# Kernel tuning notes

Measured on AMD Instinct MI355X. Metric: run time of the kernel, lower is better.

The kernel has to match this reference:

```python
import jax, jax.numpy as jnp
import numpy as np

# R-FCN PSRoI pooling constants (match init_kwargs)
P = 7          # pooled_height == pooled_width
GS = 7         # group_size
D = 21         # output_dim
SCALE = 0.0625 # spatial_scale (1/16)


def setup_inputs() -> dict:
    key = jax.random.key(0)
    k1, k2, k3, k4 = jax.random.split(key, 4)
    N, C, H, W = 4, D * GS * GS, 80, 80   # C = output_dim * group_size^2
    R = 2048
    features = jax.random.normal(k1, (N, C, H, W), dtype=jnp.float32)
    img = H / SCALE  # 1280 px image
    bidx = jax.random.randint(k2, (R,), 0, N).astype(jnp.float32)
    xy1 = jax.random.uniform(k3, (R, 2), minval=0.0, maxval=img * 0.6)
    wh = jax.random.uniform(k4, (R, 2), minval=img * 0.05, maxval=img * 0.4)
    xy2 = jnp.clip(xy1 + wh, 0.0, img - 1.0)
    rois = jnp.concatenate([bidx[:, None], xy1, xy2], axis=1)  # [R,5]: (b,x1,y1,x2,y2)
    return {"features": features, "rois": rois}


def reference(features, rois):
    """Position-sensitive RoI pooling (R-FCN psroi_pooling_forward_cuda semantics).

    Each output bin (ctop, ph, pw) averages feature channel
    c = (ctop*GS + gh)*GS + gw over the bin's integer pixel region.
    Bin sums are computed exactly via a 2D integral image, turning the
    irregular per-bin reduction into 4 gathers per bin.
    """
    N, C, H, W = features.shape
    R = rois.shape[0]

    # Integral image: ii[n,c,i,j] = sum of features[n,c,:i,:j]; shape [N,C,H+1,W+1]
    ii = jnp.pad(
        jnp.cumsum(jnp.cumsum(features, axis=2), axis=3),
        ((0, 0), (0, 0), (1, 0), (1, 0)),
    )

    b = rois[:, 0].astype(jnp.int32)                       # [R]
    x1 = jnp.round(rois[:, 1]) * SCALE
    y1 = jnp.round(rois[:, 2]) * SCALE
    x2 = (jnp.round(rois[:, 3]) + 1.0) * SCALE
    y2 = (jnp.round(rois[:, 4]) + 1.0) * SCALE
    bin_w = jnp.maximum(x2 - x1, 0.1) / P                  # [R]
    bin_h = jnp.maximum(y2 - y1, 0.1) / P

    g = jnp.arange(P, dtype=jnp.float32)                   # bin index grid
    hs = jnp.clip(jnp.floor(g[None, :] * bin_h[:, None] + y1[:, None]), 0, H).astype(jnp.int32)        # [R,P]
    he = jnp.clip(jnp.ceil((g[None, :] + 1.0) * bin_h[:, None] + y1[:, None]), 0, H).astype(jnp.int32)
    ws = jnp.clip(jnp.floor(g[None, :] * bin_w[:, None] + x1[:, None]), 0, W).astype(jnp.int32)
    we = jnp.clip(jnp.ceil((g[None, :] + 1.0) * bin_w[:, None] + x1[:, None]), 0, W).astype(jnp.int32)

    # Position-sensitive channel map: c[ctop,ph,pw] = (ctop*GS+gh)*GS+gw
    ctop = jnp.arange(D)[:, None, None]
    gh = jnp.clip((jnp.arange(P) * GS) // P, 0, GS - 1)[None, :, None]
    gw = jnp.clip((jnp.arange(P) * GS) // P, 0, GS - 1)[None, None, :]
    cmap = (ctop * GS + gh) * GS + gw                      # [D,P,P]

    # Broadcast gather indices to [R,D,P,P]
    B = b[:, None, None, None]
    Cc = cmap[None]
    HS = hs[:, None, :, None]; HE = he[:, None, :, None]
    WS = ws[:, None, None, :]; WE = we[:, None, None, :]

    s = ii[B, Cc, HE, WE] - ii[B, Cc, HS, WE] - ii[B, Cc, HE, WS] + ii[B, Cc, HS, WS]
    area = ((HE - HS) * (WE - WS)).astype(features.dtype)
    out = jnp.where(area > 0, s / jnp.maximum(area, 1.0), jnp.zeros((), features.dtype))
    return out  # [R, D, P, P]
```

## Files before the change

kernel.cpp:

```cpp
#include <hip/hip_runtime.h>

#define P   7
#define GS  7
#define D   21
#define HH  80
#define WW  80
#define CC  (D * GS * GS)
#define PLANE (HH * WW)
#define IW  84
#define NSEG 5
#define SEGLEN 16
#define NBLK 512
#define BUFQ 2048
#define BUFF (BUFQ * 4)
#define REALQ 1680

__device__ __forceinline__ float recip7() {
    union { unsigned u; float f; } c; c.u = 0x3E124925u; return c.f;
}

__device__ __forceinline__ float mul_add_nofma(float a, float b, float c) {
    float t = a * b;
    asm volatile("" : "+v"(t));
    return t + c;
}

#define MEMFENCE() asm volatile("" ::: "memory")
#define LGKM_BAR() do { asm volatile("s_waitcnt lgkmcnt(0)" ::: "memory"); \
                        __builtin_amdgcn_s_barrier(); MEMFENCE(); } while (0)

__device__ __forceinline__ void gll16(const float* g, float* l) {
    __builtin_amdgcn_global_load_lds(
        (const __attribute__((address_space(1))) void*)g,
        (__attribute__((address_space(3))) void*)l, 16, 0, 0);
}

__device__ __forceinline__ void stage_issue(const float* plane, float* buf, int tid) {
    #pragma unroll
    for (int k = 0; k < 4; ++k) {
        int q0 = (tid & ~63) + k * 512;
        int q  = q0 + (tid & 63);
        int row = q / 21, w4 = q - row * 21;
        const float* src = (q < REALQ && w4 < 20) ? (plane + row * WW + w4 * 4)
                                                  : plane;
        gll16(src, buf + q0 * 4);
    }
}

__global__ __launch_bounds__(1024) void prep_kernel(
    const float* __restrict__ rois, int R, int N,
    unsigned short* __restrict__ hshe,
    unsigned short* __restrict__ wswe,
    int* __restrict__ jlist, int* __restrict__ base)
{
    __shared__ unsigned char bsh[2048];
    __shared__ int wcnt[16][8];
    __shared__ int wbase[16][8];
    __shared__ int baseS[9];
    int tid = threadIdx.x, wave = tid >> 6, lane = tid & 63;

    for (int r = tid; r < R; r += 1024) {
        const float* roi = rois + (size_t)r * 5;
        bsh[r] = (unsigned char)(int)roi[0];

        float x1 = rintf(roi[1]) * 0.0625f;
        float y1 = rintf(roi[2]) * 0.0625f;
        float x2 = (rintf(roi[3]) + 1.0f) * 0.0625f;
        float y2 = (rintf(roi[4]) + 1.0f) * 0.0625f;
        float bin_w = fmaxf(x2 - x1, 0.1f) * recip7();
        float bin_h = fmaxf(y2 - y1, 0.1f) * recip7();
        asm volatile("" : "+v"(bin_w), "+v"(bin_h));

        #pragma unroll
        for (int g = 0; g < 7; ++g) {
            float hs_f = floorf(mul_add_nofma((float)g,       bin_h, y1));
            float he_f = ceilf (mul_add_nofma((float)(g + 1), bin_h, y1));
            float ws_f = floorf(mul_add_nofma((float)g,       bin_w, x1));
            float we_f = ceilf (mul_add_nofma((float)(g + 1), bin_w, x1));
            int hs = (int)fminf(fmaxf(hs_f, 0.0f), 80.0f);
            int he = (int)fminf(fmaxf(he_f, 0.0f), 80.0f);
            int ws = (int)fminf(fmaxf(ws_f, 0.0f), 80.0f);
            int we = (int)fminf(fmaxf(we_f, 0.0f), 80.0f);
            hshe[r * 7 + g] = (unsigned short)(hs | (he << 8));
            wswe[r * 7 + g] = (unsigned short)(ws | (we << 8));
        }
    }
    __syncthreads();

    int chunk = (R + 15) / 16;
    int rbeg = wave * chunk;
    int rend = min(rbeg + chunk, R);
    int cnt[8];
    #pragma unroll
    for (int b = 0; b < 8; ++b) cnt[b] = 0;
    for (int rr = rbeg + lane; rr < rend; rr += 64) {
        int bv = bsh[rr];
        #pragma unroll
        for (int b = 0; b < 8; ++b) {
            if (b < N) cnt[b] += __popcll(__ballot(bv == b));
        }
    }
    if (lane == 0) {
        #pragma unroll
        for (int b = 0; b < 8; ++b) wcnt[wave][b] = cnt[b];
    }
    __syncthreads();

    if (tid < 8) {
        int b = tid, acc = 0;
        for (int w = 0; w < 16; ++w) { wbase[w][b] = acc; acc += wcnt[w][b]; }
        baseS[b] = acc;
    }
    __syncthreads();
    if (tid == 0) {
        int acc = 0;
        for (int b = 0; b < N; ++b) { int t = baseS[b]; baseS[b] = acc; acc += t; }
        baseS[N] = acc;
    }
    __syncthreads();

    {
        int off[8];
        #pragma unroll
        for (int b = 0; b < 8; ++b) off[b] = (b < N) ? (baseS[b] + wbase[wave][b]) : 0;
        for (int rr = rbeg + lane; rr < rend; rr += 64) {
            int bv = bsh[rr];
            #pragma unroll
            for (int b = 0; b < 8; ++b) {
                if (b < N) {
                    unsigned long long mask = __ballot(bv == b);
                    if (bv == b) {
                        int pos = off[b] + __popcll(mask & ((1ull << lane) - 1ull));
                        jlist[pos] = rr;
                    }
                    off[b] += __popcll(mask);
                }
            }
        }
    }
    if (tid <= N) base[tid] = baseS[tid];
}

__global__ __launch_bounds__(512) void psroi_plane_kernel(
    const float* __restrict__ feat, int R, int NPLANES,
    const unsigned short* __restrict__ hshe,
    const unsigned short* __restrict__ wswe,
    const int* __restrict__ jlist, const int* __restrict__ base,
    float* __restrict__ dst)
{
    __shared__ float bufA[BUFF];
    __shared__ float bufB[BUFF];
    __shared__ float tot[NSEG][HH];

    int tid = threadIdx.x;
    int bid = blockIdx.x;

    stage_issue(feat + (size_t)bid * PLANE, bufA, tid);

    bool act = tid < NSEG * WW;
    int seg = tid / WW;
    int lw  = tid % WW;

    int parity = 0;
    for (int p = bid; p < NPLANES; p += NBLK, parity ^= 1) {
        float* ii = parity ? bufB : bufA;
        float* nx = parity ? bufA : bufB;
        int pn = p + NBLK;
        if (pn < NPLANES) {
            stage_issue(feat + (size_t)pn * PLANE, nx, tid);
            asm volatile("s_waitcnt vmcnt(4)" ::: "memory");
        } else {
            asm volatile("s_waitcnt vmcnt(0)" ::: "memory");
        }
        __builtin_amdgcn_s_barrier();
        MEMFENCE();

        int b = p / CC, c = p % CC;
        int rem = c % (GS * GS);
        int gh  = rem / GS, gw = rem % GS;
        int j0 = base[b], j1 = base[b + 1];
        int jA = j0 + tid, jB = jA + 512, jC = jA + 1024, jD = jA + 1536;
        int rA = (jA < j1) ? jlist[jA] : 0;
        int rB = (jB < j1) ? jlist[jB] : 0;
        int rC = (jC < j1) ? jlist[jC] : 0;
        int rD = (jD < j1) ? jlist[jD] : 0;
        unsigned hA = (jA < j1) ? hshe[rA * 7 + gh] : 0;
        unsigned wA = (jA < j1) ? wswe[rA * 7 + gw] : 0;
        unsigned hB = (jB < j1) ? hshe[rB * 7 + gh] : 0;
        unsigned wB = (jB < j1) ? wswe[rB * 7 + gw] : 0;
        unsigned hC = (jC < j1) ? hshe[rC * 7 + gh] : 0;
        unsigned wC = (jC < j1) ? wswe[rC * 7 + gw] : 0;
        unsigned hD = (jD < j1) ? hshe[rD * 7 + gh] : 0;
        unsigned wD = (jD < j1) ? wswe[rD * 7 + gw] : 0;

        {
            float v[SEGLEN];
            int col = lw, h0 = seg * SEGLEN;
            if (act) {
                float s = 0.0f;
                #pragma unroll
                for (int k = 0; k < SEGLEN; ++k) { v[k] = ii[(h0 + k) * IW + col]; s += v[k]; }
                tot[seg][lw] = s;
            }
            LGKM_BAR();
            if (act) {
                float off = 0.0f;
                #pragma unroll
                for (int jj = 0; jj < NSEG - 1; ++jj) if (jj < seg) off += tot[jj][lw];
                float run = off;
                #pragma unroll
                for (int k = 0; k < SEGLEN; ++k) { run += v[k]; ii[(h0 + k) * IW + col] = run; }
            }
            LGKM_BAR();
        }
        {
            float4 q0, q1, q2, q3;
            int row = lw, w0 = seg * SEGLEN;
            float4* rp = (float4*)&ii[row * IW + w0];
            if (act) {
                q0 = rp[0]; q1 = rp[1]; q2 = rp[2]; q3 = rp[3];
                float s;
                s  = q0.x; s += q0.y; s += q0.z; s += q0.w;
                s += q1.x; s += q1.y; s += q1.z; s += q1.w;
                s += q2.x; s += q2.y; s += q2.z; s += q2.w;
                s += q3.x; s += q3.y; s += q3.z; s += q3.w;
                tot[seg][row] = s;
            }
            LGKM_BAR();
            if (act) {
                float off = 0.0f;
                #pragma unroll
                for (int jj = 0; jj < NSEG - 1; ++jj) if (jj < seg) off += tot[jj][row];
                float run = off;
                run += q0.x; q0.x = run; run += q0.y; q0.y = run;
                run += q0.z; q0.z = run; run += q0.w; q0.w = run;
                run += q1.x; q1.x = run; run += q1.y; q1.y = run;
                run += q1.z; q1.z = run; run += q1.w; q1.w = run;
                run += q2.x; q2.x = run; run += q2.y; q2.y = run;
                run += q2.z; q2.z = run; run += q2.w; q2.w = run;
                run += q3.x; q3.x = run; run += q3.y; q3.y = run;
                run += q3.z; q3.z = run; run += q3.w; q3.w = run;
                rp[0] = q0; rp[1] = q1; rp[2] = q2; rp[3] = q3;
            }
            LGKM_BAR();
        }

        #define IIV(hq, wq) ( ((hq) > 0 && (wq) > 0)                              \
            ? ii[((hq) - 1) * IW + ((wq) - 1)] : 0.0f )
        #define EMIT(jX, hX, wX)                                                  \
        if (jX < j1) {                                                            \
            int hs = hX & 255, he = (int)(hX >> 8);                               \
            int ws = wX & 255, we = (int)(wX >> 8);                               \
            float s = ((IIV(he, we) - IIV(hs, we))                                \
                     -  IIV(he, ws)) + IIV(hs, ws);                               \
            int area = (he - hs) * (we - ws);                                     \
            dst[(size_t)c * R + jX] = (area > 0) ? (s / (float)area) : 0.0f;      \
        }
        EMIT(jA, hA, wA)
        EMIT(jB, hB, wB)
        EMIT(jC, hC, wC)
        EMIT(jD, hD, wD)
        #undef EMIT
        #undef IIV

        LGKM_BAR();
    }
}

__global__ __launch_bounds__(256) void transpose_kernel(
    const float* __restrict__ in, const int* __restrict__ jlist,
    float* __restrict__ out, int R, int C)
{
    __shared__ float t[64][65];
    __shared__ int rows[64];
    int j0 = blockIdx.x * 64;
    int c0 = blockIdx.y * 64;
    int tx = threadIdx.x, ty = threadIdx.y;
    int tid = ty * 64 + tx;

    if (tid < 64 && j0 + tid < R) rows[tid] = jlist[j0 + tid];

    #pragma unroll
    for (int k0 = 0; k0 < 64; k0 += 4) {
        int k = k0 + ty;
        int cc = c0 + k, jj = j0 + tx;
        if (cc < C && jj < R) t[k][tx] = in[(size_t)cc * R + jj];
    }
    __syncthreads();
    #pragma unroll
    for (int k0 = 0; k0 < 64; k0 += 4) {
        int k = k0 + ty;
        int cc = c0 + tx;
        if (j0 + k < R && cc < C) out[(size_t)rows[k] * C + cc] = t[tx][k];
    }
}

__global__ __launch_bounds__(256) void psroi_fallback_kernel(
    const float* __restrict__ feat, const float* __restrict__ rois,
    int R, float* __restrict__ out)
{
    __shared__ float ii[81 * 81];
    int bid = blockIdx.x;
    int b = bid / CC, c = bid % CC;
    int rem = c % 49, gh = rem / 7, gw = rem % 7;

    const float* plane = feat + ((size_t)b * CC + c) * PLANE;
    for (int i = threadIdx.x; i < PLANE; i += 256) {
        int h = i / WW, w = i % WW;
        ii[(h + 1) * 81 + (w + 1)] = plane[i];
    }
    for (int i = threadIdx.x; i < 81; i += 256) { ii[i] = 0.0f; ii[i * 81] = 0.0f; }
    __syncthreads();
    if (threadIdx.x < WW) {
        int w = threadIdx.x + 1; float s = 0.0f;
        for (int h = 1; h <= HH; ++h) { s += ii[h * 81 + w]; ii[h * 81 + w] = s; }
    }
    __syncthreads();
    if (threadIdx.x < HH) {
        int h = threadIdx.x + 1; float* row = &ii[h * 81]; float s = 0.0f;
        for (int w = 1; w <= WW; ++w) { s += row[w]; row[w] = s; }
    }
    __syncthreads();
    for (int r = threadIdx.x; r < R; r += 256) {
        const float* roi = rois + (size_t)r * 5;
        if ((int)roi[0] != b) continue;
        float x1 = rintf(roi[1]) * 0.0625f;
        float y1 = rintf(roi[2]) * 0.0625f;
        float x2 = (rintf(roi[3]) + 1.0f) * 0.0625f;
        float y2 = (rintf(roi[4]) + 1.0f) * 0.0625f;
        float bw = fmaxf(x2 - x1, 0.1f) * recip7();
        float bh = fmaxf(y2 - y1, 0.1f) * recip7();
        asm volatile("" : "+v"(bw), "+v"(bh));
        int hs = (int)fminf(fmaxf(floorf(mul_add_nofma((float)gh,     bh, y1)), 0.0f), 80.0f);
        int he = (int)fminf(fmaxf(ceilf (mul_add_nofma((float)(gh+1), bh, y1)), 0.0f), 80.0f);
        int ws = (int)fminf(fmaxf(floorf(mul_add_nofma((float)gw,     bw, x1)), 0.0f), 80.0f);
        int we = (int)fminf(fmaxf(ceilf (mul_add_nofma((float)(gw+1), bw, x1)), 0.0f), 80.0f);
        float s = ii[he * 81 + we] - ii[hs * 81 + we] - ii[he * 81 + ws] + ii[hs * 81 + ws];
        int area = (he - hs) * (we - ws);
        out[(size_t)r * CC + c] = (area > 0) ? (s / (float)area) : 0.0f;
    }
}

extern "C" void kernel_launch(void* const* d_in, const int* in_sizes, int n_in,
                              void* d_out, int out_size, void* d_ws, size_t ws_size,
                              hipStream_t stream)
{
    const float* feat = (const float*)d_in[0];
    const float* rois = (const float*)d_in[1];
    float* out        = (float*)d_out;

    int R = in_sizes[1] / 5;
    int N = in_sizes[0] / (CC * PLANE);
    int NPLANES = N * CC;

    size_t off_wsT  = 0;
    size_t off_hshe = (off_wsT + (size_t)CC * R * sizeof(float) + 15) & ~(size_t)15;
    size_t off_wswe = off_hshe + (size_t)R * 7 * sizeof(unsigned short);
    size_t off_jl   = (off_wswe + (size_t)R * 7 * sizeof(unsigned short) + 15) & ~(size_t)15;
    size_t off_base = off_jl + (size_t)R * sizeof(int);
    size_t need     = off_base + (size_t)(N + 1) * sizeof(int);

    bool chunk_ok = (((R + 15) / 16) % 64) == 0;

    if (ws_size >= need && N <= 8 && R <= 2048 && chunk_ok && NPLANES > NBLK) {
        char* ws = (char*)d_ws;
        float*          ws_T = (float*)(ws + off_wsT);
        unsigned short* hshe = (unsigned short*)(ws + off_hshe);
        unsigned short* wswe = (unsigned short*)(ws + off_wswe);
        int*            jl   = (int*)(ws + off_jl);
        int*            base = (int*)(ws + off_base);

        prep_kernel<<<1, 1024, 0, stream>>>(rois, R, N, hshe, wswe, jl, base);
        psroi_plane_kernel<<<NBLK, 512, 0, stream>>>(
            feat, R, NPLANES, hshe, wswe, jl, base, ws_T);
        dim3 blk(64, 4), grd((R + 63) / 64, (CC + 63) / 64);
        transpose_kernel<<<grd, blk, 0, stream>>>(ws_T, jl, out, R, CC);
    } else {
        psroi_fallback_kernel<<<NPLANES, 256, 0, stream>>>(feat, rois, R, out);
    }
}
```

Before: 51.78 us.

## Replace LDS double-buffer async loads with register prefetch and single LDS plane

Drops the two LDS plane buffers filled by global_load_lds and instead prefetches the next plane into registers during compute, writing it to a single LDS buffer after the current plane's emit phase. Halving LDS use and adding launch_bounds(512,6) aims to raise occupancy, and the persistent grid grows from 512 to 768 blocks. The cost is higher register pressure and an extra barrier plus LDS write per plane, and the global loads now cannot land directly in LDS.

After: 54.10 us. 1.04x slower.

```diff
diff --git a/kernel.cpp b/kernel.cpp
--- a/kernel.cpp
+++ b/kernel.cpp
@@ -10,10 +10,8 @@
 #define IW  84
 #define NSEG 5
 #define SEGLEN 16
-#define NBLK 512
-#define BUFQ 2048
-#define BUFF (BUFQ * 4)
-#define REALQ 1680
+#define GRIDB 768
+#define Q4N 144
 
 __device__ __forceinline__ float recip7() {
     union { unsigned u; float f; } c; c.u = 0x3E124925u; return c.f;
@@ -28,24 +26,6 @@
 #define MEMFENCE() asm volatile("" ::: "memory")
 #define LGKM_BAR() do { asm volatile("s_waitcnt lgkmcnt(0)" ::: "memory"); \
                         __builtin_amdgcn_s_barrier(); MEMFENCE(); } while (0)
-
-__device__ __forceinline__ void gll16(const float* g, float* l) {
-    __builtin_amdgcn_global_load_lds(
-        (const __attribute__((address_space(1))) void*)g,
-        (__attribute__((address_space(3))) void*)l, 16, 0, 0);
-}
-
-__device__ __forceinline__ void stage_issue(const float* plane, float* buf, int tid) {
-    #pragma unroll
-    for (int k = 0; k < 4; ++k) {
-        int q0 = (tid & ~63) + k * 512;
-        int q  = q0 + (tid & 63);
-        int row = q / 21, w4 = q - row * 21;
-        const float* src = (q < REALQ && w4 < 20) ? (plane + row * WW + w4 * 4)
-                                                  : plane;
-        gll16(src, buf + q0 * 4);
-    }
-}
 
 __global__ __launch_bounds__(1024) void prep_kernel(
     const float* __restrict__ rois, int R, int N,
@@ -141,39 +121,59 @@
     if (tid <= N) base[tid] = baseS[tid];
 }
 
-__global__ __launch_bounds__(512) void psroi_plane_kernel(
+__global__ __launch_bounds__(512, 6) void psroi_plane_kernel(
     const float* __restrict__ feat, int R, int NPLANES,
     const unsigned short* __restrict__ hshe,
     const unsigned short* __restrict__ wswe,
     const int* __restrict__ jlist, const int* __restrict__ base,
     float* __restrict__ dst)
 {
-    __shared__ float bufA[BUFF];
-    __shared__ float bufB[BUFF];
+    __shared__ float ii[HH * IW];
     __shared__ float tot[NSEG][HH];
 
     int tid = threadIdx.x;
     int bid = blockIdx.x;
-
-    stage_issue(feat + (size_t)bid * PLANE, bufA, tid);
+    bool s4 = tid < Q4N;
+
+    int q0 = tid, q1 = tid + 512, q2 = tid + 1024, q3 = tid + 1536;
+    int r0_ = q0 / 21, c40 = q0 - r0_ * 21;
+    int r1_ = q1 / 21, c41 = q1 - r1_ * 21;
+    int r2_ = q2 / 21, c42 = q2 - r2_ * 21;
+    int r3_ = q3 / 21, c43 = q3 - r3_ * 21;
+    int g0 = (c40 < 20) ? (r0_ * WW + c40 * 4) : 0;
+    int g1 = (c41 < 20) ? (r1_ * WW + c41 * 4) : 0;
+    int g2 = (c42 < 20) ? (r2_ * WW + c42 * 4) : 0;
+    int g3 = (c43 < 20) ? (r3_ * WW + c43 * 4) : 0;
 
     bool act = tid < NSEG * WW;
     int seg = tid / WW;
     int lw  = tid % WW;
 
-    int parity = 0;
-    for (int p = bid; p < NPLANES; p += NBLK, parity ^= 1) {
-        float* ii = parity ? bufB : bufA;
-        float* nx = parity ? bufA : bufB;
-        int pn = p + NBLK;
-        if (pn < NPLANES) {
-            stage_issue(feat + (size_t)pn * PLANE, nx, tid);
-            asm volatile("s_waitcnt vmcnt(4)" ::: "memory");
-        } else {
-            asm volatile("s_waitcnt vmcnt(0)" ::: "memory");
-        }
-        __builtin_amdgcn_s_barrier();
-        MEMFENCE();
+    {
+        const float* pl = feat + (size_t)bid * PLANE;
+        float4 a0 = *(const float4*)(pl + g0);
+        float4 a1 = *(const float4*)(pl + g1);
+        float4 a2 = *(const float4*)(pl + g2);
+        float4 a3 = s4 ? *(const float4*)(pl + g3) : make_float4(0, 0, 0, 0);
+        *(float4*)(ii + q0 * 4) = a0;
+        *(float4*)(ii + q1 * 4) = a1;
+        *(float4*)(ii + q2 * 4) = a2;
+        if (s4) *(float4*)(ii + q3 * 4) = a3;
+    }
+    LGKM_BAR();
+
+    for (int p = bid; p < NPLANES; p += GRIDB) {
+        int pn = p + GRIDB;
+        bool has_next = pn < NPLANES;
+
+        float4 n0, n1, n2, n3;
+        {
+            const float* pl = feat + (size_t)(has_next ? pn : p) * PLANE;
+            n0 = *(const float4*)(pl + g0);
+            n1 = *(const float4*)(pl + g1);
+            n2 = *(const float4*)(pl + g2);
+            n3 = s4 ? *(const float4*)(pl + g3) : make_float4(0, 0, 0, 0);
+        }
 
         int b = p / CC, c = p % CC;
         int rem = c % (GS * GS);
@@ -214,16 +214,16 @@
             LGKM_BAR();
         }
         {
-            float4 q0, q1, q2, q3;
-            int row = lw, w0 = seg * SEGLEN;
-            float4* rp = (float4*)&ii[row * IW + w0];
+            float4 q4a, q4b, q4c, q4d;
+            int row = lw, w0s = seg * SEGLEN;
+            float4* rp = (float4*)&ii[row * IW + w0s];
             if (act) {
-                q0 = rp[0]; q1 = rp[1]; q2 = rp[2]; q3 = rp[3];
+                q4a = rp[0]; q4b = rp[1]; q4c = rp[2]; q4d = rp[3];
                 float s;
-                s  = q0.x; s += q0.y; s += q0.z; s += q0.w;
-                s += q1.x; s += q1.y; s += q1.z; s += q1.w;
-                s += q2.x; s += q2.y; s += q2.z; s += q2.w;
-                s += q3.x; s += q3.y; s += q3.z; s += q3.w;
+                s  = q4a.x; s += q4a.y; s += q4a.z; s += q4a.w;
+                s += q4b.x; s += q4b.y; s += q4b.z; s += q4b.w;
+                s += q4c.x; s += q4c.y; s += q4c.z; s += q4c.w;
+                s += q4d.x; s += q4d.y; s += q4d.z; s += q4d.w;
                 tot[seg][row] = s;
             }
             LGKM_BAR();
@@ -232,15 +232,15 @@
                 #pragma unroll
                 for (int jj = 0; jj < NSEG - 1; ++jj) if (jj < seg) off += tot[jj][row];
                 float run = off;
-                run += q0.x; q0.x = run; run += q0.y; q0.y = run;
-                run += q0.z; q0.z = run; run += q0.w; q0.w = run;
-                run += q1.x; q1.x = run; run += q1.y; q1.y = run;
-                run += q1.z; q1.z = run; run += q1.w; q1.w = run;
-                run += q2.x; q2.x = run; run += q2.y; q2.y = run;
-                run += q2.z; q2.z = run; run += q2.w; q2.w = run;
-                run += q3.x; q3.x = run; run += q3.y; q3.y = run;
-                run += q3.z; q3.z = run; run += q3.w; q3.w = run;
-                rp[0] = q0; rp[1] = q1; rp[2] = q2; rp[3] = q3;
+                run += q4a.x; q4a.x = run; run += q4a.y; q4a.y = run;
+                run += q4a.z; q4a.z = run; run += q4a.w; q4a.w = run;
+                run += q4b.x; q4b.x = run; run += q4b.y; q4b.y = run;
+                run += q4b.z; q4b.z = run; run += q4b.w; q4b.w = run;
+                run += q4c.x; q4c.x = run; run += q4c.y; q4c.y = run;
+                run += q4c.z; q4c.z = run; run += q4c.w; q4c.w = run;
+                run += q4d.x; q4d.x = run; run += q4d.y; q4d.y = run;
+                run += q4d.z; q4d.z = run; run += q4d.w; q4d.w = run;
+                rp[0] = q4a; rp[1] = q4b; rp[2] = q4c; rp[3] = q4d;
             }
             LGKM_BAR();
         }
@@ -263,6 +263,14 @@
         #undef EMIT
         #undef IIV
 
+        LGKM_BAR();
+
+        if (has_next) {
+            *(float4*)(ii + q0 * 4) = n0;
+            *(float4*)(ii + q1 * 4) = n1;
+            *(float4*)(ii + q2 * 4) = n2;
+            if (s4) *(float4*)(ii + q3 * 4) = n3;
+        }
         LGKM_BAR();
     }
 }
@@ -362,7 +370,7 @@
 
     bool chunk_ok = (((R + 15) / 16) % 64) == 0;
 
-    if (ws_size >= need && N <= 8 && R <= 2048 && chunk_ok && NPLANES > NBLK) {
+    if (ws_size >= need && N <= 8 && R <= 2048 && chunk_ok) {
         char* ws = (char*)d_ws;
         float*          ws_T = (float*)(ws + off_wsT);
         unsigned short* hshe = (unsigned short*)(ws + off_hshe);
@@ -371,7 +379,8 @@
         int*            base = (int*)(ws + off_base);
 
         prep_kernel<<<1, 1024, 0, stream>>>(rois, R, N, hshe, wswe, jl, base);
-        psroi_plane_kernel<<<NBLK, 512, 0, stream>>>(
+        int grid = (NPLANES < GRIDB) ? NPLANES : GRIDB;
+        psroi_plane_kernel<<<grid, 512, 0, stream>>>(
             feat, R, NPLANES, hshe, wswe, jl, base, ws_T);
         dim3 blk(64, 4), grd((R + 63) / 64, (CC + 63) / 64);
         transpose_kernel<<<grd, blk, 0, stream>>>(ws_T, jl, out, R, CC);
```
